# Optimization experiments

Hardware: AMD Instinct MI355X
Metric: run time of the kernel (lower is better)

The kernel has to match this reference:

```python
import jax, jax.numpy as jnp
import numpy as np

N = 50000      # nodes
E = 1600000    # edges (avg degree 32)
FIN = 6        # input feature dim (hardcoded in GCN.__init__)
H = 128        # hidden_channels


def _lin(key, fan_in, fan_out):
    s = 1.0 / np.sqrt(fan_in)
    kw, kb = jax.random.split(key)
    W = jax.random.uniform(kw, (fan_in, fan_out), jnp.float32, -s, s)
    b = jax.random.uniform(kb, (fan_out,), jnp.float32, -s, s)
    return W, b


def setup_inputs():
    key = jax.random.key(0)
    ks = jax.random.split(key, 8)
    x = jax.random.normal(ks[0], (N, FIN), jnp.float32)
    edge_index = jax.random.randint(ks[1], (2, E), 0, N, dtype=jnp.int32)
    W0, b0 = _lin(ks[2], FIN, H)
    W1, b1 = _lin(ks[3], H, H)
    W2, b2 = _lin(ks[4], H, H)
    Rw0, Rb0 = _lin(ks[5], H, H)
    Rw1, Rb1 = _lin(ks[6], H, H)
    Rw2, Rb2 = _lin(ks[7], H, 1)
    return {"x": x, "edge_index": edge_index,
            "W0": W0, "b0": b0, "W1": W1, "b1": b1, "W2": W2, "b2": b2,
            "Rw0": Rw0, "Rb0": Rb0, "Rw1": Rw1, "Rb1": Rb1, "Rw2": Rw2, "Rb2": Rb2}


def reference(x, edge_index, W0, b0, W1, b1, W2, b2, Rw0, Rb0, Rw1, Rb1, Rw2, Rb2):
    n = x.shape[0]
    loop = jnp.arange(n, dtype=edge_index.dtype)
    src = jnp.concatenate([edge_index[0], loop])   # add self-loops (PyG GCNConv default)
    dst = jnp.concatenate([edge_index[1], loop])
    # symmetric normalization D^{-1/2} (A+I) D^{-1/2}, degrees from in-edges incl. self-loops
    deg = jax.ops.segment_sum(jnp.ones_like(dst, jnp.float32), dst, num_segments=n)
    dinv = jnp.where(deg > 0.0, jax.lax.rsqrt(deg), 0.0)
    norm = dinv[src] * dinv[dst]                   # [E+N]

    def conv(h, W, b):
        h = h @ W                                  # linear transform first (PyG GCNConv)
        msg = h[src] * norm[:, None]               # gather + normalize, [E+N, H]
        return jax.ops.segment_sum(msg, dst, num_segments=n) + b  # scatter-add + bias

    h = jax.nn.relu(conv(x, W0, b0))
    h = jax.nn.relu(conv(h, W1, b1))
    h = jax.nn.relu(conv(h, W2, b2))
    h = jax.nn.leaky_relu(h @ Rw0 + Rb0, 0.01)
    h = jax.nn.leaky_relu(h @ Rw1 + Rb1, 0.01)
    return h @ Rw2 + Rb2                           # [N, 1]
```

## Files before the change

### kernel.cpp

```cpp
#include <hip/hip_runtime.h>


#define HDIM 128
#define NB1 128

typedef __attribute__((ext_vector_type(8))) short bf16x8;
typedef __attribute__((ext_vector_type(4))) float f32x4;
typedef __attribute__((ext_vector_type(2))) float f32x2;

__device__ inline unsigned short bf16rn(float f) {
  unsigned u = __float_as_uint(f);
  unsigned r = (u + 0x7FFFu + ((u >> 16) & 1u)) >> 16;
  return (unsigned short)r;
}
__device__ inline float bf16tof(unsigned short h) {
  return __uint_as_float(((unsigned)h) << 16);
}
__device__ inline unsigned char fp8enc(float f) {
  return (unsigned char)(__builtin_amdgcn_cvt_pk_fp8_f32(f, f, 0, false) & 0xFF);
}


__global__ __launch_bounds__(256) void chunk_sums_kernel(const int* __restrict__ in,
                                                         int* __restrict__ sums, int M) {
  int i = blockIdx.x * 256 + threadIdx.x;
  int v = (i < M) ? in[i] : 0;
#pragma unroll
  for (int d = 1; d < 64; d <<= 1) v += __shfl_xor(v, d, 64);
  __shared__ int ws[4];
  int lane = threadIdx.x & 63, wid = threadIdx.x >> 6;
  if (lane == 0) ws[wid] = v;
  __syncthreads();
  if (threadIdx.x == 0) sums[blockIdx.x] = ws[0] + ws[1] + ws[2] + ws[3];
}

__global__ __launch_bounds__(256) void small_scan_kernel(const int* __restrict__ in,
                                                         int* __restrict__ outv, int M) {
  __shared__ int wsum[4];
  __shared__ int carry_s;
  int tid = threadIdx.x, lane = tid & 63, wid = tid >> 6;
  if (tid == 0) carry_s = 0;
  __syncthreads();
  int nchunks = (M + 4095) / 4096;
  for (int c = 0; c < nchunks; ++c) {
    int base = c * 4096 + tid * 16;
    int v[16];
#pragma unroll
    for (int j = 0; j < 16; ++j) {
      int i = base + j;
      v[j] = (i < M) ? in[i] : 0;
    }
    int s = 0;
#pragma unroll
    for (int j = 0; j < 16; ++j) { int t = v[j]; v[j] = s; s += t; }
    int tot = s;
    int inc = tot;
#pragma unroll
    for (int d = 1; d < 64; d <<= 1) {
      int t = __shfl_up(inc, (unsigned)d, 64);
      if (lane >= d) inc += t;
    }
    if (lane == 63) wsum[wid] = inc;
    int texcl = inc - tot;
    __syncthreads();
    int wexcl = 0, ctot = 0;
#pragma unroll
    for (int w = 0; w < 4; ++w) {
      int ws = wsum[w];
      if (w < wid) wexcl += ws;
      ctot += ws;
    }
    int cbase = carry_s + wexcl + texcl;
#pragma unroll
    for (int j = 0; j < 16; ++j) {
      int i = base + j;
      if (i < M) outv[i] = cbase + v[j];
    }
    __syncthreads();
    if (tid == 0) carry_s += ctot;
    __syncthreads();
  }
}

__global__ __launch_bounds__(256) void write_scan_kernel(const int* __restrict__ in,
                                                         const int* __restrict__ bases,
                                                         int* __restrict__ outv, int M) {
  int i = blockIdx.x * 256 + threadIdx.x;
  int v = (i < M) ? in[i] : 0;
  int lane = threadIdx.x & 63, wid = threadIdx.x >> 6;
  int inc = v;
#pragma unroll
  for (int d = 1; d < 64; d <<= 1) {
    int t = __shfl_up(inc, (unsigned)d, 64);
    if (lane >= d) inc += t;
  }
  __shared__ int ws[4];
  if (lane == 63) ws[wid] = inc;
  __syncthreads();
  int woff = 0;
  for (int w = 0; w < wid; ++w) woff += ws[w];
  inc += woff;
  int base = bases[blockIdx.x];
  if (i < M) outv[i] = base + inc - v;
}


__global__ __launch_bounds__(1024) void bucket_hist(const int* __restrict__ ei, int E,
                                                    int chunk, int* __restrict__ gh, int nbk) {
  __shared__ int h[1024];
  int tid = threadIdx.x, b = blockIdx.x;
  for (int i = tid; i < nbk; i += 1024) h[i] = 0;
  __syncthreads();
  int s = b * chunk, e = min(E, s + chunk);
  for (int i = s + tid; i < e; i += 1024) atomicAdd(&h[ei[E + i] >> 6], 1);
  __syncthreads();
  for (int k = tid; k < nbk; k += 1024) gh[k * NB1 + b] = h[k];
}

__global__ __launch_bounds__(1024) void bucket_place(const int* __restrict__ ei, int E,
                                                     int chunk, const int* __restrict__ ghs,
                                                     int2* __restrict__ tmp, int nbk) {
  __shared__ int cur[1024];
  int tid = threadIdx.x, b = blockIdx.x;
  for (int k = tid; k < nbk; k += 1024) cur[k] = ghs[k * NB1 + b];
  __syncthreads();
  int s = b * chunk, e = min(E, s + chunk);
  for (int i = s + tid; i < e; i += 1024) {
    int src = ei[i], dst = ei[E + i];
    int pos = atomicAdd(&cur[dst >> 6], 1);
    tmp[pos] = make_int2(src, dst);
  }
}

__global__ __launch_bounds__(256) void fine_count(const int2* __restrict__ tmp,
                                                  const int* __restrict__ ghs,
                                                  int* __restrict__ off,
                                                  float* __restrict__ dinv,
                                                  int n, int E, int nbk) {
  __shared__ int cnt[64][4];
  int tid = threadIdx.x, k = blockIdx.x;
  ((int*)cnt)[tid] = 0;
  int e0 = ghs[k * NB1];
  int e1 = (k + 1 < nbk) ? ghs[(k + 1) * NB1] : E;
  __syncthreads();
  for (int i = e0 + tid; i < e1; i += 256)
    atomicAdd(&cnt[tmp[i].y & 63][tid & 3], 1);
  __syncthreads();
  if (tid < 64) {
    int c = cnt[tid][0] + cnt[tid][1] + cnt[tid][2] + cnt[tid][3];
    int inc = c;
#pragma unroll
    for (int d = 1; d < 64; d <<= 1) {
      int t = __shfl_up(inc, (unsigned)d, 64);
      if (tid >= d) inc += t;
    }
    int node = k * 64 + tid;
    if (node < n) {
      off[node] = e0 + inc - c;
      dinv[node] = rsqrtf((float)(c + 1));
      if (node == n - 1) off[n] = e0 + inc;
    }
  }
}

__global__ __launch_bounds__(256) void fine_sort(const int2* __restrict__ tmp,
                                                 const int* __restrict__ off,
                                                 const int* __restrict__ ghs,
                                                 const float* __restrict__ dinv,
                                                 int2* __restrict__ recs,
                                                 int n, int E, int nbk) {
  __shared__ int cur[64];
  int tid = threadIdx.x, k = blockIdx.x;
  if (tid < 64) {
    int node = k * 64 + tid;
    cur[tid] = (node < n) ? off[node] : 0;
  }
  int e0 = ghs[k * NB1];
  int e1 = (k + 1 < nbk) ? ghs[(k + 1) * NB1] : E;
  __syncthreads();
  for (int i = e0 + tid; i < e1; i += 256) {
    int2 t = tmp[i];
    int pos = atomicAdd(&cur[t.y & 63], 1);
    float w = dinv[t.x] * dinv[t.y];
    recs[pos] = make_int2(t.x, __float_as_int(w));
  }
}

__global__ void prop6_kernel(const float* __restrict__ x, const int* __restrict__ off,
                             const int2* __restrict__ recs,
                             const float* __restrict__ dinv, float* __restrict__ aggx, int n) {
  int g = (blockIdx.x * blockDim.x + threadIdx.x) >> 3;
  int l = threadIdx.x & 7;
  if (g >= n) return;
  float di = dinv[g];
  float acc = 0.f;
  if (l < 6) acc = di * di * x[g * 6 + l];
  int e0 = off[g], e1 = off[g + 1];
  int e = e0;
  for (; e + 4 <= e1; e += 4) {
    int2 r0 = recs[e], r1 = recs[e + 1], r2 = recs[e + 2], r3 = recs[e + 3];
    float u0 = 0.f, u1 = 0.f, u2 = 0.f, u3 = 0.f;
    if (l < 6) {
      u0 = x[r0.x * 6 + l]; u1 = x[r1.x * 6 + l];
      u2 = x[r2.x * 6 + l]; u3 = x[r3.x * 6 + l];
    }
    acc += __int_as_float(r0.y) * u0 + __int_as_float(r1.y) * u1 +
           __int_as_float(r2.y) * u2 + __int_as_float(r3.y) * u3;
  }
  for (; e < e1; ++e) {
    int2 r = recs[e];
    if (l < 6) acc += __int_as_float(r.y) * x[r.x * 6 + l];
  }
  if (l < 6) aggx[g * 6 + l] = acc;
}

__global__ __launch_bounds__(256) void gemm0_kernel(const float* __restrict__ aggx,
                                                    const float* __restrict__ W0,
                                                    const float* __restrict__ b0,
                                                    unsigned short* __restrict__ out, int n) {
  __shared__ float Ws[6 * 128];
  __shared__ float bs[128];
  for (int i = threadIdx.x; i < 6 * 128; i += 256) Ws[i] = W0[i];
  if (threadIdx.x < 128) bs[threadIdx.x] = b0[threadIdx.x];
  __syncthreads();
  int f = threadIdx.x & 127;
  int h = threadIdx.x >> 7;
  int base = blockIdx.x * 16;
#pragma unroll
  for (int j = 0; j < 8; ++j) {
    int nd = base + h * 8 + j;
    if (nd < n) {
      float acc = bs[f];
#pragma unroll
      for (int k = 0; k < 6; ++k) acc += aggx[nd * 6 + k] * Ws[k * 128 + f];
      out[(size_t)nd * HDIM + f] = bf16rn(fmaxf(acc, 0.f));
    }
  }
}

__global__ __launch_bounds__(256) void wprep_kernel(const float* __restrict__ w1,
                                                    const float* __restrict__ w2,
                                                    const float* __restrict__ rw0,
                                                    const float* __restrict__ rw1,
                                                    unsigned short* __restrict__ wtf) {
  int widx = blockIdx.y;
  const float* W = (widx == 0) ? w1 : (widx == 1) ? w2 : (widx == 2) ? rw0 : rw1;
  int c = blockIdx.x * 256 + threadIdx.x;
  int l = c & 63, kk = (c >> 6) & 3, ft = c >> 8;
  int f = ft * 16 + (l & 15);
  int k0 = kk * 32 + ((l >> 4) << 3);
  unsigned short v[8];
#pragma unroll
  for (int j = 0; j < 8; ++j) v[j] = bf16rn(W[(size_t)(k0 + j) * 128 + f]);
  uint4 pk;
  pk.x = (unsigned)v[0] | ((unsigned)v[1] << 16);
  pk.y = (unsigned)v[2] | ((unsigned)v[3] << 16);
  pk.z = (unsigned)v[4] | ((unsigned)v[5] << 16);
  pk.w = (unsigned)v[6] | ((unsigned)v[7] << 16);
  *(uint4*)&wtf[((size_t)widx * 16384) + (size_t)c * 8] = pk;
}

__global__ __launch_bounds__(256) void mgemm_kernel(const unsigned short* __restrict__ in,
                                                    const unsigned short* __restrict__ wtf,
                                                    unsigned char* __restrict__ out8, int n) {
  __shared__ unsigned short Alds[8192];
  __shared__ unsigned short Wlds[16384];
  int tid = threadIdx.x;
  int rowBase = blockIdx.x * 64;
  {
    const uint4* src = (const uint4*)wtf;
    uint4* dst = (uint4*)Wlds;
#pragma unroll
    for (int c = 0; c < 8; ++c) dst[c * 256 + tid] = src[c * 256 + tid];
  }
  {
    int k8 = tid & 15, tr = tid >> 4;
#pragma unroll
    for (int c = 0; c < 4; ++c) {
      int row = tr + c * 16;
      int gr = rowBase + row;
      uint4 v = make_uint4(0u, 0u, 0u, 0u);
      if (gr < n) v = *(const uint4*)&in[(size_t)gr * HDIM + k8 * 8];
      int srow = row ^ (k8 & 7);
      *(uint4*)&Alds[k8 * 512 + srow * 8] = v;
    }
  }
  __syncthreads();
  int wv = tid >> 6, lane = tid & 63;
  int l16 = lane >> 4, fcol = lane & 15;
  int lrow = wv * 16 + fcol;
  bf16x8 af[4];
#pragma unroll
  for (int kk = 0; kk < 4; ++kk) {
    int k8 = kk * 4 + l16;
    int srow = lrow ^ (k8 & 7);
    af[kk] = *(const bf16x8*)&Alds[k8 * 512 + srow * 8];
  }
  f32x4 acc[8];
#pragma unroll
  for (int ft = 0; ft < 8; ++ft) acc[ft] = (f32x4)(0.f);
#pragma unroll
  for (int ft = 0; ft < 8; ++ft) {
#pragma unroll
    for (int kk = 0; kk < 4; ++kk) {
      bf16x8 bfr = *(const bf16x8*)&Wlds[(((ft * 4 + kk) * 64) + lane) * 8];
      acc[ft] = __builtin_amdgcn_mfma_f32_16x16x32_bf16(af[kk], bfr, acc[ft], 0, 0, 0);
    }
  }
  int orow0 = rowBase + wv * 16 + l16 * 4;
#pragma unroll
  for (int ft = 0; ft < 8; ++ft) {
    int f = ft * 16 + fcol;
#pragma unroll
    for (int r = 0; r < 4; ++r) {
      int row = orow0 + r;
      if (row < n) out8[(size_t)row * HDIM + f] = fp8enc(acc[ft][r]);
    }
  }
}

__global__ __launch_bounds__(256) void mgemm_head(const unsigned short* __restrict__ in,
                                                  const unsigned short* __restrict__ wtf0,
                                                  const unsigned short* __restrict__ wtf1,
                                                  const float* __restrict__ b0,
                                                  const float* __restrict__ b1,
                                                  const float* __restrict__ rw2,
                                                  const float* __restrict__ rb2,
                                                  float* __restrict__ out1, int n) {
  __shared__ unsigned short Wlds0[16384];
  __shared__ unsigned short Wlds1[16384];
  __shared__ unsigned short Alds[8192];
  int tid = threadIdx.x;
  int rowBase = blockIdx.x * 64;
  {
    const uint4* s0 = (const uint4*)wtf0;
    const uint4* s1 = (const uint4*)wtf1;
    uint4* d0 = (uint4*)Wlds0;
    uint4* d1 = (uint4*)Wlds1;
#pragma unroll
    for (int c = 0; c < 8; ++c) {
      d0[c * 256 + tid] = s0[c * 256 + tid];
      d1[c * 256 + tid] = s1[c * 256 + tid];
    }
  }
  {
    int k8 = tid & 15, tr = tid >> 4;
#pragma unroll
    for (int c = 0; c < 4; ++c) {
      int row = tr + c * 16;
      int gr = rowBase + row;
      uint4 v = make_uint4(0u, 0u, 0u, 0u);
      if (gr < n) v = *(const uint4*)&in[(size_t)gr * HDIM + k8 * 8];
      int srow = row ^ (k8 & 7);
      *(uint4*)&Alds[k8 * 512 + srow * 8] = v;
    }
  }
  __syncthreads();
  int wv = tid >> 6, lane = tid & 63;
  int l16 = lane >> 4, fcol = lane & 15;
  int lrow = wv * 16 + fcol;
  bf16x8 af[4];
#pragma unroll
  for (int kk = 0; kk < 4; ++kk) {
    int k8 = kk * 4 + l16;
    int srow = lrow ^ (k8 & 7);
    af[kk] = *(const bf16x8*)&Alds[k8 * 512 + srow * 8];
  }
  __syncthreads();
  f32x4 acc[8];
#pragma unroll
  for (int ft = 0; ft < 8; ++ft) acc[ft] = (f32x4)(0.f);
#pragma unroll
  for (int ft = 0; ft < 8; ++ft) {
#pragma unroll
    for (int kk = 0; kk < 4; ++kk) {
      bf16x8 bfr = *(const bf16x8*)&Wlds0[(((ft * 4 + kk) * 64) + lane) * 8];
      acc[ft] = __builtin_amdgcn_mfma_f32_16x16x32_bf16(af[kk], bfr, acc[ft], 0, 0, 0);
    }
  }
  int brow0 = wv * 16 + l16 * 4;
#pragma unroll
  for (int ft = 0; ft < 8; ++ft) {
    int f = ft * 16 + fcol;
    float bb = b0[f];
    int k8 = f >> 3, elem = f & 7;
#pragma unroll
    for (int r = 0; r < 4; ++r) {
      float v = acc[ft][r] + bb;
      v = v > 0.f ? v : 0.01f * v;
      int row = brow0 + r;
      int srow = row ^ (k8 & 7);
      Alds[k8 * 512 + srow * 8 + elem] = bf16rn(v);
    }
  }
  __syncthreads();
  bf16x8 bf2[4];
#pragma unroll
  for (int kk = 0; kk < 4; ++kk) {
    int k8 = kk * 4 + l16;
    int srow = lrow ^ (k8 & 7);
    bf2[kk] = *(const bf16x8*)&Alds[k8 * 512 + srow * 8];
  }
  f32x4 acc2[8];
#pragma unroll
  for (int ft = 0; ft < 8; ++ft) acc2[ft] = (f32x4)(0.f);
#pragma unroll
  for (int ft = 0; ft < 8; ++ft) {
#pragma unroll
    for (int kk = 0; kk < 4; ++kk) {
      bf16x8 bfr = *(const bf16x8*)&Wlds1[(((ft * 4 + kk) * 64) + lane) * 8];
      acc2[ft] = __builtin_amdgcn_mfma_f32_16x16x32_bf16(bf2[kk], bfr, acc2[ft], 0, 0, 0);
    }
  }
  int orow0 = rowBase + wv * 16 + l16 * 4;
  float p[4] = {0.f, 0.f, 0.f, 0.f};
#pragma unroll
  for (int ft = 0; ft < 8; ++ft) {
    int f = ft * 16 + fcol;
    float bb = b1[f], ww = rw2[f];
#pragma unroll
    for (int r = 0; r < 4; ++r) {
      float v = acc2[ft][r] + bb;
      v = v > 0.f ? v : 0.01f * v;
      p[r] += v * ww;
    }
  }
#pragma unroll
  for (int d = 1; d < 16; d <<= 1) {
#pragma unroll
    for (int r = 0; r < 4; ++r) p[r] += __shfl_xor(p[r], d, 64);
  }
  if (fcol == 0) {
    float rb = rb2[0];
#pragma unroll
    for (int r = 0; r < 4; ++r) {
      int row = orow0 + r;
      if (row < n) out1[row] = p[r] + rb;
    }
  }
}

__global__ __launch_bounds__(256) void aggregate_kernel(const unsigned char* __restrict__ t8,
                                                        const int* __restrict__ off,
                                                        const int2* __restrict__ recs,
                                                        const float* __restrict__ dinv,
                                                        const float* __restrict__ bias,
                                                        unsigned short* __restrict__ out, int n) {
  int wave = (blockIdx.x * blockDim.x + threadIdx.x) >> 6;
  int half = (threadIdx.x >> 5) & 1;
  int lane32 = threadIdx.x & 31;
  int node = wave * 2 + half;
  if (node >= n) return;
  const unsigned* tf = (const unsigned*)t8;
  float di = dinv[node];
  float self = di * di;
  unsigned v = tf[(size_t)node * 32 + lane32];
  f32x2 vlo = __builtin_amdgcn_cvt_pk_f32_fp8(v, false);
  f32x2 vhi = __builtin_amdgcn_cvt_pk_f32_fp8(v, true);
  float a0 = self * vlo[0], a1 = self * vlo[1];
  float a2 = self * vhi[0], a3 = self * vhi[1];
  int e0 = off[node], e1 = off[node + 1];
  int e = e0;
  for (; e + 8 <= e1; e += 8) {
    int2 r[8];
    unsigned u[8];
#pragma unroll
    for (int j = 0; j < 8; ++j) r[j] = recs[e + j];
#pragma unroll
    for (int j = 0; j < 8; ++j) u[j] = tf[(size_t)r[j].x * 32 + lane32];
#pragma unroll
    for (int j = 0; j < 8; ++j) {
      float w = __int_as_float(r[j].y);
      f32x2 lo = __builtin_amdgcn_cvt_pk_f32_fp8(u[j], false);
      f32x2 hi = __builtin_amdgcn_cvt_pk_f32_fp8(u[j], true);
      a0 += w * lo[0]; a1 += w * lo[1];
      a2 += w * hi[0]; a3 += w * hi[1];
    }
  }
  for (; e < e1; ++e) {
    int2 r = recs[e];
    float w = __int_as_float(r.y);
    unsigned u = tf[(size_t)r.x * 32 + lane32];
    f32x2 lo = __builtin_amdgcn_cvt_pk_f32_fp8(u, false);
    f32x2 hi = __builtin_amdgcn_cvt_pk_f32_fp8(u, true);
    a0 += w * lo[0]; a1 += w * lo[1];
    a2 += w * hi[0]; a3 += w * hi[1];
  }
  float4 b = *((const float4*)bias + lane32);
  a0 = fmaxf(a0 + b.x, 0.f);
  a1 = fmaxf(a1 + b.y, 0.f);
  a2 = fmaxf(a2 + b.z, 0.f);
  a3 = fmaxf(a3 + b.w, 0.f);
  ushort4 o;
  o.x = bf16rn(a0); o.y = bf16rn(a1); o.z = bf16rn(a2); o.w = bf16rn(a3);
  *((ushort4*)out + (size_t)node * 32 + lane32) = o;
}


static inline size_t align256(size_t x) { return (x + 255) & ~(size_t)255; }

extern "C" void kernel_launch(void* const* d_in, const int* in_sizes, int n_in,
                              void* d_out, int out_size, void* d_ws, size_t ws_size,
                              hipStream_t stream) {
  const float* x   = (const float*)d_in[0];
  const int*   ei  = (const int*)d_in[1];
  const float* W0  = (const float*)d_in[2];
  const float* b0  = (const float*)d_in[3];
  const float* W1  = (const float*)d_in[4];
  const float* b1  = (const float*)d_in[5];
  const float* W2  = (const float*)d_in[6];
  const float* b2  = (const float*)d_in[7];
  const float* Rw0 = (const float*)d_in[8];
  const float* Rb0 = (const float*)d_in[9];
  const float* Rw1 = (const float*)d_in[10];
  const float* Rb1 = (const float*)d_in[11];
  const float* Rw2 = (const float*)d_in[12];
  const float* Rb2 = (const float*)d_in[13];
  float* out = (float*)d_out;

  int N = in_sizes[0] / 6;
  int E = in_sizes[1] / 2;
  int NBK = (N + 63) >> 6;
  int M = NBK * NB1;
  int MB = (M + 255) / 256;
  int chunk = (E + NB1 - 1) / NB1;

  char* p = (char*)d_ws;
  size_t o = 0;
  int* off     = (int*)(p + o); o = align256(o + (size_t)(N + 1) * 4);
  float* dinv  = (float*)(p + o); o = align256(o + (size_t)N * 4);
  int* bsums   = (int*)(p + o); o = align256(o + (size_t)MB * 4);
  int* bscan   = (int*)(p + o); o = align256(o + (size_t)MB * 4);
  int* gh      = (int*)(p + o); o = align256(o + (size_t)M * 4);
  int* ghs     = (int*)(p + o); o = align256(o + (size_t)M * 4);
  int2* tmp    = (int2*)(p + o); o = align256(o + (size_t)E * 8);
  int2* recs   = (int2*)(p + o); o = align256(o + (size_t)E * 8);
  float* aggx  = (float*)(p + o); o = align256(o + (size_t)N * 6 * 4);
  unsigned short* Wtf = (unsigned short*)(p + o); o = align256(o + (size_t)4 * 16384 * 2);
  unsigned short* H0  = (unsigned short*)(p + o); o = align256(o + (size_t)N * HDIM * 2);
  unsigned char*  H1  = (unsigned char*)(p + o); o = align256(o + (size_t)N * HDIM);
  (void)ws_size;

  bucket_hist<<<NB1, 1024, 0, stream>>>(ei, E, chunk, gh, NBK);
  chunk_sums_kernel<<<MB, 256, 0, stream>>>(gh, bsums, M);
  small_scan_kernel<<<1, 256, 0, stream>>>(bsums, bscan, MB);
  write_scan_kernel<<<MB, 256, 0, stream>>>(gh, bscan, ghs, M);
  bucket_place<<<NB1, 1024, 0, stream>>>(ei, E, chunk, ghs, tmp, NBK);
  fine_count<<<NBK, 256, 0, stream>>>(tmp, ghs, off, dinv, N, E, NBK);
  fine_sort<<<NBK, 256, 0, stream>>>(tmp, off, ghs, dinv, recs, N, E, NBK);

  {
    dim3 g(8, 4);
    wprep_kernel<<<g, 256, 0, stream>>>(W1, W2, Rw0, Rw1, Wtf);
  }

  prop6_kernel<<<(N + 31) / 32, 256, 0, stream>>>(x, off, recs, dinv, aggx, N);
  gemm0_kernel<<<(N + 15) / 16, 256, 0, stream>>>(aggx, W0, b0, H0, N);

  int mGrid = (N + 63) / 64;
  int aggGrid = (N + 7) / 8;

  mgemm_kernel<<<mGrid, 256, 0, stream>>>(H0, Wtf + 0 * 16384, H1, N);
  aggregate_kernel<<<aggGrid, 256, 0, stream>>>(H1, off, recs, dinv, b1, H0, N);
  mgemm_kernel<<<mGrid, 256, 0, stream>>>(H0, Wtf + 1 * 16384, H1, N);
  aggregate_kernel<<<aggGrid, 256, 0, stream>>>(H1, off, recs, dinv, b2, H0, N);
  mgemm_head<<<mGrid, 256, 0, stream>>>(H0, Wtf + 2 * 16384, Wtf + 3 * 16384,
                                        Rb0, Rb1, Rw2, Rb2, out, N);
}
```

Baseline: 194.7 us.

## Factor GCN normalization into source prescale and destination scale; drop per-edge weights

Splits the symmetric D^-1/2 normalization so sources are prescaled by dinv (in the GEMM epilogue or a small prescale kernel) and destinations are scaled after aggregation. The CSR records shrink from (src, weight) pairs to plain source indices, which halves index traffic in every aggregation pass. The fine count and fine sort kernels are also merged into one, with edges staged in LDS. This adds a tiny prescale kernel, and scaling before fp8 encoding changes the rounding behaviour.

```diff
diff --git a/kernel.cpp b/kernel.cpp
--- a/kernel.cpp
+++ b/kernel.cpp
@@ -3,6 +3,7 @@
 
 #define HDIM 128
 #define NB1 128
+#define SCAP 4096
 
 typedef __attribute__((ext_vector_type(8))) short bf16x8;
 typedef __attribute__((ext_vector_type(4))) float f32x4;
@@ -132,19 +133,29 @@
   }
 }
 
-__global__ __launch_bounds__(256) void fine_count(const int2* __restrict__ tmp,
+__global__ __launch_bounds__(256) void fine_build(const int2* __restrict__ tmp,
                                                   const int* __restrict__ ghs,
                                                   int* __restrict__ off,
                                                   float* __restrict__ dinv,
+                                                  int* __restrict__ recs,
                                                   int n, int E, int nbk) {
+  __shared__ int2 stage[SCAP];
   __shared__ int cnt[64][4];
+  __shared__ int cur[64];
   int tid = threadIdx.x, k = blockIdx.x;
-  ((int*)cnt)[tid] = 0;
+  ((int*)cnt)[tid & 255] = 0;
   int e0 = ghs[k * NB1];
   int e1 = (k + 1 < nbk) ? ghs[(k + 1) * NB1] : E;
-  __syncthreads();
-  for (int i = e0 + tid; i < e1; i += 256)
-    atomicAdd(&cnt[tmp[i].y & 63][tid & 3], 1);
+  int cntE = e1 - e0;
+  int nst = cntE < SCAP ? cntE : SCAP;
+  __syncthreads();
+  for (int i = tid; i < nst; i += 256) {
+    int2 t = tmp[e0 + i];
+    stage[i] = t;
+    atomicAdd(&cnt[t.y & 63][tid & 3], 1);
+  }
+  for (int i = nst + tid; i < cntE; i += 256)
+    atomicAdd(&cnt[tmp[e0 + i].y & 63][tid & 3], 1);
   __syncthreads();
   if (tid < 64) {
     int c = cnt[tid][0] + cnt[tid][1] + cnt[tid][2] + cnt[tid][3];
@@ -157,61 +168,53 @@
     int node = k * 64 + tid;
     if (node < n) {
       off[node] = e0 + inc - c;
+      cur[tid] = e0 + inc - c;
       dinv[node] = rsqrtf((float)(c + 1));
       if (node == n - 1) off[n] = e0 + inc;
-    }
-  }
-}
-
-__global__ __launch_bounds__(256) void fine_sort(const int2* __restrict__ tmp,
-                                                 const int* __restrict__ off,
-                                                 const int* __restrict__ ghs,
-                                                 const float* __restrict__ dinv,
-                                                 int2* __restrict__ recs,
-                                                 int n, int E, int nbk) {
-  __shared__ int cur[64];
-  int tid = threadIdx.x, k = blockIdx.x;
-  if (tid < 64) {
-    int node = k * 64 + tid;
-    cur[tid] = (node < n) ? off[node] : 0;
-  }
-  int e0 = ghs[k * NB1];
-  int e1 = (k + 1 < nbk) ? ghs[(k + 1) * NB1] : E;
-  __syncthreads();
-  for (int i = e0 + tid; i < e1; i += 256) {
-    int2 t = tmp[i];
+    } else {
+      cur[tid] = 0;
+    }
+  }
+  __syncthreads();
+  for (int i = tid; i < nst; i += 256) {
+    int2 t = stage[i];
     int pos = atomicAdd(&cur[t.y & 63], 1);
-    float w = dinv[t.x] * dinv[t.y];
-    recs[pos] = make_int2(t.x, __float_as_int(w));
-  }
-}
-
-__global__ void prop6_kernel(const float* __restrict__ x, const int* __restrict__ off,
-                             const int2* __restrict__ recs,
+    recs[pos] = t.x;
+  }
+  for (int i = nst + tid; i < cntE; i += 256) {
+    int2 t = tmp[e0 + i];
+    int pos = atomicAdd(&cur[t.y & 63], 1);
+    recs[pos] = t.x;
+  }
+}
+
+
+__global__ void xprescale_kernel(const float* __restrict__ x, const float* __restrict__ dinv,
+                                 float* __restrict__ xp, int n) {
+  int i = blockIdx.x * blockDim.x + threadIdx.x;
+  if (i < n * 6) xp[i] = x[i] * dinv[i / 6];
+}
+
+__global__ void prop6_kernel(const float* __restrict__ xp, const int* __restrict__ off,
+                             const int* __restrict__ recs,
                              const float* __restrict__ dinv, float* __restrict__ aggx, int n) {
   int g = (blockIdx.x * blockDim.x + threadIdx.x) >> 3;
   int l = threadIdx.x & 7;
   if (g >= n) return;
-  float di = dinv[g];
   float acc = 0.f;
-  if (l < 6) acc = di * di * x[g * 6 + l];
+  if (l < 6) acc = xp[g * 6 + l];
   int e0 = off[g], e1 = off[g + 1];
   int e = e0;
   for (; e + 4 <= e1; e += 4) {
-    int2 r0 = recs[e], r1 = recs[e + 1], r2 = recs[e + 2], r3 = recs[e + 3];
-    float u0 = 0.f, u1 = 0.f, u2 = 0.f, u3 = 0.f;
-    if (l < 6) {
-      u0 = x[r0.x * 6 + l]; u1 = x[r1.x * 6 + l];
-      u2 = x[r2.x * 6 + l]; u3 = x[r3.x * 6 + l];
-    }
-    acc += __int_as_float(r0.y) * u0 + __int_as_float(r1.y) * u1 +
-           __int_as_float(r2.y) * u2 + __int_as_float(r3.y) * u3;
+    int s0 = recs[e], s1 = recs[e + 1], s2 = recs[e + 2], s3 = recs[e + 3];
+    if (l < 6)
+      acc += xp[s0 * 6 + l] + xp[s1 * 6 + l] + xp[s2 * 6 + l] + xp[s3 * 6 + l];
   }
   for (; e < e1; ++e) {
-    int2 r = recs[e];
-    if (l < 6) acc += __int_as_float(r.y) * x[r.x * 6 + l];
-  }
-  if (l < 6) aggx[g * 6 + l] = acc;
+    int s = recs[e];
+    if (l < 6) acc += xp[s * 6 + l];
+  }
+  if (l < 6) aggx[g * 6 + l] = dinv[g] * acc;
 }
 
 __global__ __launch_bounds__(256) void gemm0_kernel(const float* __restrict__ aggx,
@@ -262,6 +265,7 @@
 
 __global__ __launch_bounds__(256) void mgemm_kernel(const unsigned short* __restrict__ in,
                                                     const unsigned short* __restrict__ wtf,
+                                                    const float* __restrict__ dinv,
                                                     unsigned char* __restrict__ out8, int n) {
   __shared__ unsigned short Alds[8192];
   __shared__ unsigned short Wlds[16384];
@@ -308,13 +312,19 @@
     }
   }
   int orow0 = rowBase + wv * 16 + l16 * 4;
+  float dv[4];
+#pragma unroll
+  for (int r = 0; r < 4; ++r) {
+    int row = orow0 + r;
+    dv[r] = (row < n) ? dinv[row] : 0.f;
+  }
 #pragma unroll
   for (int ft = 0; ft < 8; ++ft) {
     int f = ft * 16 + fcol;
 #pragma unroll
     for (int r = 0; r < 4; ++r) {
       int row = orow0 + r;
-      if (row < n) out8[(size_t)row * HDIM + f] = fp8enc(acc[ft][r]);
+      if (row < n) out8[(size_t)row * HDIM + f] = fp8enc(dv[r] * acc[ft][r]);
     }
   }
 }
@@ -442,7 +452,7 @@
 
 __global__ __launch_bounds__(256) void aggregate_kernel(const unsigned char* __restrict__ t8,
                                                         const int* __restrict__ off,
-                                                        const int2* __restrict__ recs,
+                                                        const int* __restrict__ recs,
                                                         const float* __restrict__ dinv,
                                                         const float* __restrict__ bias,
                                                         unsigned short* __restrict__ out, int n) {
@@ -452,45 +462,38 @@
   int node = wave * 2 + half;
   if (node >= n) return;
   const unsigned* tf = (const unsigned*)t8;
-  float di = dinv[node];
-  float self = di * di;
   unsigned v = tf[(size_t)node * 32 + lane32];
   f32x2 vlo = __builtin_amdgcn_cvt_pk_f32_fp8(v, false);
   f32x2 vhi = __builtin_amdgcn_cvt_pk_f32_fp8(v, true);
-  float a0 = self * vlo[0], a1 = self * vlo[1];
-  float a2 = self * vhi[0], a3 = self * vhi[1];
+  float a0 = vlo[0], a1 = vlo[1], a2 = vhi[0], a3 = vhi[1];
   int e0 = off[node], e1 = off[node + 1];
   int e = e0;
   for (; e + 8 <= e1; e += 8) {
-    int2 r[8];
+    int s[8];
     unsigned u[8];
 #pragma unroll
-    for (int j = 0; j < 8; ++j) r[j] = recs[e + j];
-#pragma unroll
-    for (int j = 0; j < 8; ++j) u[j] = tf[(size_t)r[j].x * 32 + lane32];
+    for (int j = 0; j < 8; ++j) s[j] = recs[e + j];
+#pragma unroll
+    for (int j = 0; j < 8; ++j) u[j] = tf[(size_t)s[j] * 32 + lane32];
 #pragma unroll
     for (int j = 0; j < 8; ++j) {
-      float w = __int_as_float(r[j].y);
       f32x2 lo = __builtin_amdgcn_cvt_pk_f32_fp8(u[j], false);
       f32x2 hi = __builtin_amdgcn_cvt_pk_f32_fp8(u[j], true);
-      a0 += w * lo[0]; a1 += w * lo[1];
-      a2 += w * hi[0]; a3 += w * hi[1];
+      a0 += lo[0]; a1 += lo[1]; a2 += hi[0]; a3 += hi[1];
     }
   }
   for (; e < e1; ++e) {
-    int2 r = recs[e];
-    float w = __int_as_float(r.y);
-    unsigned u = tf[(size_t)r.x * 32 + lane32];
+    unsigned u = tf[(size_t)recs[e] * 32 + lane32];
     f32x2 lo = __builtin_amdgcn_cvt_pk_f32_fp8(u, false);
     f32x2 hi = __builtin_amdgcn_cvt_pk_f32_fp8(u, true);
-    a0 += w * lo[0]; a1 += w * lo[1];
-    a2 += w * hi[0]; a3 += w * hi[1];
-  }
+    a0 += lo[0]; a1 += lo[1]; a2 += hi[0]; a3 += hi[1];
+  }
+  float di = dinv[node];
   float4 b = *((const float4*)bias + lane32);
-  a0 = fmaxf(a0 + b.x, 0.f);
-  a1 = fmaxf(a1 + b.y, 0.f);
-  a2 = fmaxf(a2 + b.z, 0.f);
-  a3 = fmaxf(a3 + b.w, 0.f);
+  a0 = fmaxf(di * a0 + b.x, 0.f);
+  a1 = fmaxf(di * a1 + b.y, 0.f);
+  a2 = fmaxf(di * a2 + b.z, 0.f);
+  a3 = fmaxf(di * a3 + b.w, 0.f);
   ushort4 o;
   o.x = bf16rn(a0); o.y = bf16rn(a1); o.z = bf16rn(a2); o.w = bf16rn(a3);
   *((ushort4*)out + (size_t)node * 32 + lane32) = o;
@@ -534,7 +537,8 @@
   int* gh      = (int*)(p + o); o = align256(o + (size_t)M * 4);
   int* ghs     = (int*)(p + o); o = align256(o + (size_t)M * 4);
   int2* tmp    = (int2*)(p + o); o = align256(o + (size_t)E * 8);
-  int2* recs   = (int2*)(p + o); o = align256(o + (size_t)E * 8);
+  int* recs    = (int*)(p + o); o = align256(o + (size_t)E * 4);
+  float* xp    = (float*)(p + o); o = align256(o + (size_t)N * 6 * 4);
   float* aggx  = (float*)(p + o); o = align256(o + (size_t)N * 6 * 4);
   unsigned short* Wtf = (unsigned short*)(p + o); o = align256(o + (size_t)4 * 16384 * 2);
   unsigned short* H0  = (unsigned short*)(p + o); o = align256(o + (size_t)N * HDIM * 2);
@@ -546,23 +550,23 @@
   small_scan_kernel<<<1, 256, 0, stream>>>(bsums, bscan, MB);
   write_scan_kernel<<<MB, 256, 0, stream>>>(gh, bscan, ghs, M);
   bucket_place<<<NB1, 1024, 0, stream>>>(ei, E, chunk, ghs, tmp, NBK);
-  fine_count<<<NBK, 256, 0, stream>>>(tmp, ghs, off, dinv, N, E, NBK);
-  fine_sort<<<NBK, 256, 0, stream>>>(tmp, off, ghs, dinv, recs, N, E, NBK);
+  fine_build<<<NBK, 256, 0, stream>>>(tmp, ghs, off, dinv, recs, N, E, NBK);
 
   {
     dim3 g(8, 4);
     wprep_kernel<<<g, 256, 0, stream>>>(W1, W2, Rw0, Rw1, Wtf);
   }
 
-  prop6_kernel<<<(N + 31) / 32, 256, 0, stream>>>(x, off, recs, dinv, aggx, N);
+  xprescale_kernel<<<(N * 6 + 255) / 256, 256, 0, stream>>>(x, dinv, xp, N);
+  prop6_kernel<<<(N + 31) / 32, 256, 0, stream>>>(xp, off, recs, dinv, aggx, N);
   gemm0_kernel<<<(N + 15) / 16, 256, 0, stream>>>(aggx, W0, b0, H0, N);
 
   int mGrid = (N + 63) / 64;
   int aggGrid = (N + 7) / 8;
 
-  mgemm_kernel<<<mGrid, 256, 0, stream>>>(H0, Wtf + 0 * 16384, H1, N);
+  mgemm_kernel<<<mGrid, 256, 0, stream>>>(H0, Wtf + 0 * 16384, dinv, H1, N);
   aggregate_kernel<<<aggGrid, 256, 0, stream>>>(H1, off, recs, dinv, b1, H0, N);
-  mgemm_kernel<<<mGrid, 256, 0, stream>>>(H0, Wtf + 1 * 16384, H1, N);
+  mgemm_kernel<<<mGrid, 256, 0, stream>>>(H0, Wtf + 1 * 16384, dinv, H1, N);
   aggregate_kernel<<<aggGrid, 256, 0, stream>>>(H1, off, recs, dinv, b2, H0, N);
   mgemm_head<<<mGrid, 256, 0, stream>>>(H0, Wtf + 2 * 16384, Wtf + 3 * 16384,
                                         Rb0, Rb1, Rw2, Rb2, out, N);
```

Measured after the change: 190.7 us. 2.1% less time.
